# Performance work log

Measured on AMD Instinct MI355X. Metric: run time of the kernel, lower is better.

## Reference

```python
import jax, jax.numpy as jnp
import numpy as np

D_IN, D_K, D_V = 768, 128, 768


def setup_inputs() -> dict:
    key = jax.random.key(0)
    ks = jax.random.split(key, 7)
    x = jax.random.normal(ks[0], (4, 2048, D_IN), dtype=jnp.float32)
    s_in = 1.0 / np.sqrt(D_IN)
    Wq = jax.random.uniform(ks[1], (D_IN, D_K), minval=-s_in, maxval=s_in, dtype=jnp.float32)
    bq = jax.random.uniform(ks[2], (D_K,), minval=-s_in, maxval=s_in, dtype=jnp.float32)
    Wk = jax.random.uniform(ks[3], (D_IN, D_K), minval=-s_in, maxval=s_in, dtype=jnp.float32)
    bk = jax.random.uniform(ks[4], (D_K,), minval=-s_in, maxval=s_in, dtype=jnp.float32)
    Wv = jax.random.uniform(ks[5], (D_IN, D_V), minval=-s_in, maxval=s_in, dtype=jnp.float32)
    bv = jax.random.uniform(ks[6], (D_V,), minval=-s_in, maxval=s_in, dtype=jnp.float32)
    return {"x": x, "Wq": Wq, "bq": bq, "Wk": Wk, "bk": bk, "Wv": Wv, "bv": bv}


def reference(x, Wq, bq, Wk, bk, Wv, bv):
    # q,k: [b,t,d_k]; v: [b,t,d_v]
    q = jnp.einsum('bti,ik->btk', x, Wq) + bq
    k = jnp.einsum('bti,ik->btk', x, Wk) + bk
    v = jnp.einsum('bti,iv->btv', x, Wv) + bv
    scale = 1.0 / jnp.sqrt(jnp.asarray(D_K, dtype=jnp.float32))
    scores = jnp.einsum('bqk,btk->bqt', q, k) * scale  # [b,t,t]
    attn = jax.nn.softmax(scores, axis=-1)
    return jnp.einsum('bqt,btv->bqv', attn, v)
```

## Files before the change

### kernel.cpp

```cpp
#include <hip/hip_runtime.h>
#include <stdint.h>

typedef unsigned short u16;
typedef __attribute__((ext_vector_type(8))) short short8;
typedef __attribute__((ext_vector_type(4))) float f32x4;

#define BATCH 4
#define SEQ   2048
#define DIN   768
#define DK    128
#define DV    768
#define MTOT  (BATCH*SEQ)
#define NQKV  1024

__device__ __forceinline__ u16 f2bf(float f) {
  union { float f; uint32_t u; } v; v.f = f;
  uint32_t r = v.u + 0x7FFFu + ((v.u >> 16) & 1u);
  return (u16)(r >> 16);
}
__device__ __forceinline__ float bf2f(u16 h) {
  union { uint32_t u; float f; } v; v.u = ((uint32_t)h) << 16;
  return v.f;
}

__global__ void pack_bias(const float* __restrict__ bq, const float* __restrict__ bk,
                          const float* __restrict__ bv, float* __restrict__ biasP) {
  const float qs = 0.088388347648318447f;
  int n = blockIdx.x * 256 + threadIdx.x;
  if (n >= NQKV) return;
  biasP[n] = (n < DK) ? bq[n] * qs : (n < 2*DK ? bk[n - DK] : bv[n - 2*DK]);
}

__global__ __launch_bounds__(256) void pack_weight_t(const float* __restrict__ W,
                                                     u16* __restrict__ dst, int ldw, float sc) {
  __shared__ u16 tile[64][72];
  int i0 = blockIdx.x * 64;
  int n0 = blockIdx.y * 64;
  int tid = threadIdx.x;
  int tr = tid >> 2;
  int tc = (tid & 3) * 16;
  const float* src = W + (size_t)(i0 + tr) * ldw + n0 + tc;
  u16 o[16];
#pragma unroll
  for (int u = 0; u < 16; u += 4) {
    float4 v = *(const float4*)(src + u);
    o[u] = f2bf(v.x * sc); o[u+1] = f2bf(v.y * sc); o[u+2] = f2bf(v.z * sc); o[u+3] = f2bf(v.w * sc);
  }
  *(uint4*)&tile[tr][tc]     = *(const uint4*)&o[0];
  *(uint4*)&tile[tr][tc + 8] = *(const uint4*)&o[8];
  __syncthreads();
  u16 tmp[16];
#pragma unroll
  for (int u = 0; u < 16; ++u) tmp[u] = tile[tc + u][tr];
  u16* d = dst + (size_t)(n0 + tr) * DIN + i0 + tc;
  *(uint4*)d       = *(const uint4*)&tmp[0];
  *(uint4*)(d + 8) = *(const uint4*)&tmp[8];
}

__global__ void convert_x(const float* __restrict__ x, u16* __restrict__ xb) {
  int i = (blockIdx.x * blockDim.x + threadIdx.x) * 4;
  float4 v = *(const float4*)(x + i);
  u16 o[4] = { f2bf(v.x), f2bf(v.y), f2bf(v.z), f2bf(v.w) };
  *(uint2*)(xb + i) = *(const uint2*)o;
}

template<int MODE, int NJ>
__global__ __launch_bounds__(512, 4) void gemm_nt(
    const u16* __restrict__ A, int lda, long long sA,
    const u16* __restrict__ BT, int ldb, long long sB,
    void* __restrict__ C0, void* __restrict__ C1, int ldc, long long sC,
    int K, int gx, int gy, const float* __restrict__ bias,
    const float* __restrict__ rsum)
{
  __shared__ u16 As[2][128][64];
  __shared__ u16 Bs[2][NJ * 64][64];
  const int tid = threadIdx.x;
  const int l   = tid & 63;
  const int wid = tid >> 6;
  const int wm  = wid >> 2;
  const int wn  = wid & 3;

  const int nwg = gridDim.x;
  const int cpx = nwg >> 3;
  const int bid = blockIdx.x;
  const int wg  = (bid & 7) * cpx + (bid >> 3);
  const int z   = wg / (gx * gy);
  const int rem = wg - z * gx * gy;
  const int by  = rem / gx;
  const int bx  = rem - by * gx;
  const int m0  = bx * 128;
  const int n0  = by * (NJ * 64);

  A  += (size_t)z * (size_t)sA;
  BT += (size_t)z * (size_t)sB;

  f32x4 acc[4][NJ] = {};

  const int lr = l >> 3;
  const int lc = ((l & 7) ^ lr) * 8;

  const int CH = 2 + NJ;
  const int ca = wid * CH;
  auto STAGE = [&](int buf, int k0) {
#pragma unroll
    for (int i = 0; i < CH; ++i) {
      int c = ca + i;
      if (c < 16) {
        const u16* src = A + (size_t)(m0 + c * 8 + lr) * lda + k0 + lc;
        __builtin_amdgcn_global_load_lds(
            (const __attribute__((address_space(1))) unsigned int*)src,
            (__attribute__((address_space(3))) unsigned int*)&As[buf][c * 8][0],
            16, 0, 0);
      } else {
        int cb = c - 16;
        const u16* src = BT + (size_t)(n0 + cb * 8 + lr) * ldb + k0 + lc;
        __builtin_amdgcn_global_load_lds(
            (const __attribute__((address_space(1))) unsigned int*)src,
            (__attribute__((address_space(3))) unsigned int*)&Bs[buf][cb * 8][0],
            16, 0, 0);
      }
    }
  };

  STAGE(0, 0);
  __syncthreads();

  int cur = 0;
  for (int k0 = 0; k0 < K; k0 += 64) {
    if (k0 + 64 < K) STAGE(cur ^ 1, k0 + 64);
#pragma unroll
    for (int ks = 0; ks < 2; ++ks) {
      short8 af[4], bg[NJ];
#pragma unroll
      for (int i = 0; i < 4; ++i) {
        int row  = wm * 64 + i * 16 + (l & 15);
        int slot = (ks * 4 + (l >> 4)) ^ (row & 7);
        af[i] = *(const short8*)&As[cur][row][slot * 8];
      }
#pragma unroll
      for (int j = 0; j < NJ; ++j) {
        int row  = wn * (NJ * 16) + j * 16 + (l & 15);
        int slot = (ks * 4 + (l >> 4)) ^ (row & 7);
        bg[j] = *(const short8*)&Bs[cur][row][slot * 8];
      }
#pragma unroll
      for (int i = 0; i < 4; ++i)
#pragma unroll
        for (int j = 0; j < NJ; ++j)
          acc[i][j] = __builtin_amdgcn_mfma_f32_16x16x32_bf16(af[i], bg[j], acc[i][j], 0, 0, 0);
    }
    __syncthreads();
    cur ^= 1;
  }

  const int rbase = (l >> 4) * 4;
  const int cl    = l & 15;
#pragma unroll
  for (int i = 0; i < 4; ++i) {
#pragma unroll
    for (int j = 0; j < NJ; ++j) {
      int col = n0 + wn * (NJ * 16) + j * 16 + cl;
      int row0 = m0 + wm * 64 + i * 16 + rbase;
      if (MODE == 0) {
#pragma unroll
        for (int q = 0; q < 4; ++q) {
          float rs = rsum[(size_t)z * SEQ + row0 + q];
          ((float*)C0)[(size_t)z * (size_t)sC + (size_t)(row0 + q) * ldc + col] = acc[i][j][q] * rs;
        }
      } else if (MODE == 1) {
#pragma unroll
        for (int q = 0; q < 4; ++q)
          ((u16*)C0)[(size_t)z * (size_t)sC + (size_t)(row0 + q) * ldc + col] = f2bf(__expf(acc[i][j][q]));
      } else {
        float bv_ = bias[col];
        if (n0 < 256) {
#pragma unroll
          for (int q = 0; q < 4; ++q)
            ((u16*)C0)[(size_t)(row0 + q) * 256 + col] = f2bf(acc[i][j][q] + bv_);
        } else {
          int b = row0 >> 11, t = row0 & 2047;
          u16 o[4];
#pragma unroll
          for (int q = 0; q < 4; ++q) o[q] = f2bf(acc[i][j][q] + bv_);
          *(uint2*)&((u16*)C1)[((size_t)b * DV + (col - 256)) * SEQ + t] = *(const uint2*)o;
        }
      }
    }
  }
}

__global__ __launch_bounds__(256) void rowsum_inv(const u16* __restrict__ P, float* __restrict__ rinv) {
  int row = blockIdx.x * 4 + (threadIdx.x >> 6);
  int l   = threadIdx.x & 63;
  const u16* p = P + (size_t)row * SEQ;
  float s = 0.0f;
#pragma unroll
  for (int c = 0; c < 4; ++c) {
    uint4 d = *(const uint4*)(p + l * 8 + c * 512);
    const u16* u = (const u16*)&d;
#pragma unroll
    for (int e = 0; e < 8; ++e) s += bf2f(u[e]);
  }
#pragma unroll
  for (int sft = 32; sft; sft >>= 1) s += __shfl_xor(s, sft, 64);
  if (l == 0) rinv[row] = 1.0f / s;
}

extern "C" void kernel_launch(void* const* d_in, const int* in_sizes, int n_in,
                              void* d_out, int out_size, void* d_ws, size_t ws_size,
                              hipStream_t stream) {
  const float* x  = (const float*)d_in[0];
  const float* Wq = (const float*)d_in[1];
  const float* bq = (const float*)d_in[2];
  const float* Wk = (const float*)d_in[3];
  const float* bk = (const float*)d_in[4];
  const float* Wv = (const float*)d_in[5];
  const float* bv = (const float*)d_in[6];
  float* out = (float*)d_out;

  size_t off = 0;
  auto alloc = [&](size_t bytes) -> void* {
    void* p = (char*)d_ws + off;
    off += (bytes + 255) & ~(size_t)255;
    return p;
  };
  u16*   xb    = (u16*)alloc((size_t)MTOT * DIN * 2);
  u16*   WbT   = (u16*)alloc((size_t)NQKV * DIN * 2);
  float* biasP = (float*)alloc(NQKV * 4);
  u16*   qk    = (u16*)alloc((size_t)MTOT * 256 * 2);
  u16*   vT    = (u16*)alloc((size_t)BATCH * DV * SEQ * 2);
  u16*   P     = (u16*)alloc((size_t)BATCH * SEQ * SEQ * 2);
  float* rinv  = (float*)alloc((size_t)MTOT * 4);
  if (off > ws_size) return;

  const float qs = 0.088388347648318447f;

  pack_bias<<<dim3(4), dim3(256), 0, stream>>>(bq, bk, bv, biasP);
  pack_weight_t<<<dim3(DIN/64, DK/64), dim3(256), 0, stream>>>(Wq, WbT, DK, qs);
  pack_weight_t<<<dim3(DIN/64, DK/64), dim3(256), 0, stream>>>(Wk, WbT + (size_t)DK*DIN, DK, 1.0f);
  pack_weight_t<<<dim3(DIN/64, DV/64), dim3(256), 0, stream>>>(Wv, WbT + (size_t)2*DK*DIN, DV, 1.0f);
  convert_x<<<dim3((MTOT * DIN / 4) / 256), dim3(256), 0, stream>>>(x, xb);

  gemm_nt<2, 2><<<dim3(64 * 8), dim3(512), 0, stream>>>(
      xb, DIN, 0, WbT, DIN, 0, qk, vT, 0, 0, DIN, 64, 8, biasP, nullptr);

  gemm_nt<1, 2><<<dim3(16 * 16 * BATCH), dim3(512), 0, stream>>>(
      qk, 256, (long long)SEQ * 256,
      qk + DK, 256, (long long)SEQ * 256,
      P, nullptr, SEQ, (long long)SEQ * SEQ, DK, 16, 16, nullptr, nullptr);

  rowsum_inv<<<dim3(MTOT / 4), dim3(256), 0, stream>>>(P, rinv);

  gemm_nt<0, 3><<<dim3(16 * 4 * BATCH), dim3(512), 0, stream>>>(
      P, SEQ, (long long)SEQ * SEQ,
      vT, SEQ, (long long)DV * SEQ,
      out, nullptr, DV, (long long)SEQ * DV, SEQ, 16, 4, nullptr, rinv);
}
```

Before: 98.72 us.

## Fold softmax row sums into PV GEMM via ones-MFMA and merge pack kernels

Drops the separate rowsum_inv pass over the P matrix. Row sums are now computed inside the PV GEMM by an extra MFMA against a vector of bf16 ones, and the output is normalised in the epilogue. The QK^T exp step gets its own single-shot kernel that loads the full K=128 tile without double buffering. The three weight-pack launches and the bias-pack launch are merged into one kernel. The intent is to avoid re-reading the 32MB P buffer and to cut launch overhead, at the cost of extra MFMA work in the main GEMM.

```diff
diff --git a/kernel.cpp b/kernel.cpp
--- a/kernel.cpp
+++ b/kernel.cpp
@@ -23,20 +23,25 @@
   return v.f;
 }
 
-__global__ void pack_bias(const float* __restrict__ bq, const float* __restrict__ bk,
-                          const float* __restrict__ bv, float* __restrict__ biasP) {
+__global__ __launch_bounds__(256) void pack_all(
+    const float* __restrict__ Wq, const float* __restrict__ bq,
+    const float* __restrict__ Wk, const float* __restrict__ bk,
+    const float* __restrict__ Wv, const float* __restrict__ bv,
+    u16* __restrict__ WbT, float* __restrict__ biasP) {
   const float qs = 0.088388347648318447f;
-  int n = blockIdx.x * 256 + threadIdx.x;
-  if (n >= NQKV) return;
-  biasP[n] = (n < DK) ? bq[n] * qs : (n < 2*DK ? bk[n - DK] : bv[n - 2*DK]);
-}
-
-__global__ __launch_bounds__(256) void pack_weight_t(const float* __restrict__ W,
-                                                     u16* __restrict__ dst, int ldw, float sc) {
   __shared__ u16 tile[64][72];
+  int y = blockIdx.y;
+  const float* W; u16* dst; int ldw, nb; float sc;
+  if (y < 2)      { W = Wq; dst = WbT;                       ldw = DK; sc = qs;   nb = y;     }
+  else if (y < 4) { W = Wk; dst = WbT + (size_t)DK * DIN;    ldw = DK; sc = 1.0f; nb = y - 2; }
+  else            { W = Wv; dst = WbT + (size_t)2*DK * DIN;  ldw = DV; sc = 1.0f; nb = y - 4; }
   int i0 = blockIdx.x * 64;
-  int n0 = blockIdx.y * 64;
+  int n0 = nb * 64;
   int tid = threadIdx.x;
+  if (blockIdx.x == 0 && y == 0) {
+    for (int n = tid; n < NQKV; n += 256)
+      biasP[n] = (n < DK) ? bq[n] * qs : (n < 2*DK ? bk[n - DK] : bv[n - 2*DK]);
+  }
   int tr = tid >> 2;
   int tc = (tid & 3) * 16;
   const float* src = W + (size_t)(i0 + tr) * ldw + n0 + tc;
@@ -69,8 +74,7 @@
     const u16* __restrict__ A, int lda, long long sA,
     const u16* __restrict__ BT, int ldb, long long sB,
     void* __restrict__ C0, void* __restrict__ C1, int ldc, long long sC,
-    int K, int gx, int gy, const float* __restrict__ bias,
-    const float* __restrict__ rsum)
+    int K, int gx, int gy, const float* __restrict__ bias)
 {
   __shared__ u16 As[2][128][64];
   __shared__ u16 Bs[2][NJ * 64][64];
@@ -95,6 +99,8 @@
   BT += (size_t)z * (size_t)sB;
 
   f32x4 acc[4][NJ] = {};
+  f32x4 accO[4] = {};
+  const short8 kOnes = {16256,16256,16256,16256,16256,16256,16256,16256};
 
   const int lr = l >> 3;
   const int lc = ((l & 7) ^ lr) * 8;
@@ -148,6 +154,11 @@
 #pragma unroll
         for (int j = 0; j < NJ; ++j)
           acc[i][j] = __builtin_amdgcn_mfma_f32_16x16x32_bf16(af[i], bg[j], acc[i][j], 0, 0, 0);
+      if (MODE == 0) {
+#pragma unroll
+        for (int i = 0; i < 4; ++i)
+          accO[i] = __builtin_amdgcn_mfma_f32_16x16x32_bf16(af[i], kOnes, accO[i], 0, 0, 0);
+      }
     }
     __syncthreads();
     cur ^= 1;
@@ -157,20 +168,19 @@
   const int cl    = l & 15;
 #pragma unroll
   for (int i = 0; i < 4; ++i) {
+    f32x4 rs;
+    if (MODE == 0) {
+#pragma unroll
+      for (int q = 0; q < 4; ++q) rs[q] = 1.0f / accO[i][q];
+    }
 #pragma unroll
     for (int j = 0; j < NJ; ++j) {
       int col = n0 + wn * (NJ * 16) + j * 16 + cl;
       int row0 = m0 + wm * 64 + i * 16 + rbase;
       if (MODE == 0) {
 #pragma unroll
-        for (int q = 0; q < 4; ++q) {
-          float rs = rsum[(size_t)z * SEQ + row0 + q];
-          ((float*)C0)[(size_t)z * (size_t)sC + (size_t)(row0 + q) * ldc + col] = acc[i][j][q] * rs;
-        }
-      } else if (MODE == 1) {
-#pragma unroll
         for (int q = 0; q < 4; ++q)
-          ((u16*)C0)[(size_t)z * (size_t)sC + (size_t)(row0 + q) * ldc + col] = f2bf(__expf(acc[i][j][q]));
+          ((float*)C0)[(size_t)z * (size_t)sC + (size_t)(row0 + q) * ldc + col] = acc[i][j][q] * rs[q];
       } else {
         float bv_ = bias[col];
         if (n0 < 256) {
@@ -189,21 +199,93 @@
   }
 }
 
-__global__ __launch_bounds__(256) void rowsum_inv(const u16* __restrict__ P, float* __restrict__ rinv) {
-  int row = blockIdx.x * 4 + (threadIdx.x >> 6);
-  int l   = threadIdx.x & 63;
-  const u16* p = P + (size_t)row * SEQ;
-  float s = 0.0f;
-#pragma unroll
-  for (int c = 0; c < 4; ++c) {
-    uint4 d = *(const uint4*)(p + l * 8 + c * 512);
-    const u16* u = (const u16*)&d;
-#pragma unroll
-    for (int e = 0; e < 8; ++e) s += bf2f(u[e]);
-  }
-#pragma unroll
-  for (int sft = 32; sft; sft >>= 1) s += __shfl_xor(s, sft, 64);
-  if (l == 0) rinv[row] = 1.0f / s;
+__global__ __launch_bounds__(512, 4) void sgemm_exp(
+    const u16* __restrict__ qk, u16* __restrict__ P)
+{
+  __shared__ u16 As[128][128];
+  __shared__ u16 Bs[128][128];
+  const int tid = threadIdx.x;
+  const int l   = tid & 63;
+  const int wid = tid >> 6;
+  const int wm  = wid >> 2;
+  const int wn  = wid & 3;
+
+  const int nwg = gridDim.x;
+  const int cpx = nwg >> 3;
+  const int bid = blockIdx.x;
+  const int wg  = (bid & 7) * cpx + (bid >> 3);
+  const int z   = wg >> 8;
+  const int rem = wg & 255;
+  const int by  = rem >> 4;
+  const int bx  = rem & 15;
+  const int m0  = bx * 128;
+  const int n0  = by * 128;
+
+  const u16* A  = qk + (size_t)z * SEQ * 256;
+  const u16* BT = qk + DK + (size_t)z * SEQ * 256;
+
+  const int rin  = l >> 4;
+  const int s16  = l & 15;
+#pragma unroll
+  for (int i = 0; i < 8; ++i) {
+    int c = wid * 8 + i;
+    if (c < 32) {
+      int r = c * 4 + rin;
+      int gs = s16 ^ (r & 7);
+      const u16* src = A + (size_t)(m0 + r) * 256 + gs * 8;
+      __builtin_amdgcn_global_load_lds(
+          (const __attribute__((address_space(1))) unsigned int*)src,
+          (__attribute__((address_space(3))) unsigned int*)&As[c * 4][0],
+          16, 0, 0);
+    } else {
+      int cb = c - 32;
+      int r = cb * 4 + rin;
+      int gs = s16 ^ (r & 7);
+      const u16* src = BT + (size_t)(n0 + r) * 256 + gs * 8;
+      __builtin_amdgcn_global_load_lds(
+          (const __attribute__((address_space(1))) unsigned int*)src,
+          (__attribute__((address_space(3))) unsigned int*)&Bs[cb * 4][0],
+          16, 0, 0);
+    }
+  }
+  __syncthreads();
+
+  f32x4 acc[4][2] = {};
+#pragma unroll
+  for (int ks = 0; ks < 4; ++ks) {
+    short8 af[4], bg[2];
+#pragma unroll
+    for (int i = 0; i < 4; ++i) {
+      int row  = wm * 64 + i * 16 + (l & 15);
+      int slot = (ks * 4 + (l >> 4)) ^ (row & 7);
+      af[i] = *(const short8*)&As[row][slot * 8];
+    }
+#pragma unroll
+    for (int j = 0; j < 2; ++j) {
+      int row  = wn * 32 + j * 16 + (l & 15);
+      int slot = (ks * 4 + (l >> 4)) ^ (row & 7);
+      bg[j] = *(const short8*)&Bs[row][slot * 8];
+    }
+#pragma unroll
+    for (int i = 0; i < 4; ++i)
+#pragma unroll
+      for (int j = 0; j < 2; ++j)
+        acc[i][j] = __builtin_amdgcn_mfma_f32_16x16x32_bf16(af[i], bg[j], acc[i][j], 0, 0, 0);
+  }
+
+  const int rbase = (l >> 4) * 4;
+  const int cl    = l & 15;
+  u16* Pz = P + (size_t)z * SEQ * SEQ;
+#pragma unroll
+  for (int i = 0; i < 4; ++i)
+#pragma unroll
+    for (int j = 0; j < 2; ++j) {
+      int col  = n0 + wn * 32 + j * 16 + cl;
+      int row0 = m0 + wm * 64 + i * 16 + rbase;
+#pragma unroll
+      for (int q = 0; q < 4; ++q)
+        Pz[(size_t)(row0 + q) * SEQ + col] = f2bf(__expf(acc[i][j][q]));
+    }
 }
 
 extern "C" void kernel_launch(void* const* d_in, const int* in_sizes, int n_in,
@@ -230,29 +312,18 @@
   u16*   qk    = (u16*)alloc((size_t)MTOT * 256 * 2);
   u16*   vT    = (u16*)alloc((size_t)BATCH * DV * SEQ * 2);
   u16*   P     = (u16*)alloc((size_t)BATCH * SEQ * SEQ * 2);
-  float* rinv  = (float*)alloc((size_t)MTOT * 4);
   if (off > ws_size) return;
 
-  const float qs = 0.088388347648318447f;
-
-  pack_bias<<<dim3(4), dim3(256), 0, stream>>>(bq, bk, bv, biasP);
-  pack_weight_t<<<dim3(DIN/64, DK/64), dim3(256), 0, stream>>>(Wq, WbT, DK, qs);
-  pack_weight_t<<<dim3(DIN/64, DK/64), dim3(256), 0, stream>>>(Wk, WbT + (size_t)DK*DIN, DK, 1.0f);
-  pack_weight_t<<<dim3(DIN/64, DV/64), dim3(256), 0, stream>>>(Wv, WbT + (size_t)2*DK*DIN, DV, 1.0f);
+  pack_all<<<dim3(DIN/64, 16), dim3(256), 0, stream>>>(Wq, bq, Wk, bk, Wv, bv, WbT, biasP);
   convert_x<<<dim3((MTOT * DIN / 4) / 256), dim3(256), 0, stream>>>(x, xb);
 
   gemm_nt<2, 2><<<dim3(64 * 8), dim3(512), 0, stream>>>(
-      xb, DIN, 0, WbT, DIN, 0, qk, vT, 0, 0, DIN, 64, 8, biasP, nullptr);
-
-  gemm_nt<1, 2><<<dim3(16 * 16 * BATCH), dim3(512), 0, stream>>>(
-      qk, 256, (long long)SEQ * 256,
-      qk + DK, 256, (long long)SEQ * 256,
-      P, nullptr, SEQ, (long long)SEQ * SEQ, DK, 16, 16, nullptr, nullptr);
-
-  rowsum_inv<<<dim3(MTOT / 4), dim3(256), 0, stream>>>(P, rinv);
+      xb, DIN, 0, WbT, DIN, 0, qk, vT, 0, 0, DIN, 64, 8, biasP);
+
+  sgemm_exp<<<dim3(16 * 16 * BATCH), dim3(512), 0, stream>>>(qk, P);
 
   gemm_nt<0, 3><<<dim3(16 * 4 * BATCH), dim3(512), 0, stream>>>(
       P, SEQ, (long long)SEQ * SEQ,
       vT, SEQ, (long long)DV * SEQ,
-      out, nullptr, DV, (long long)SEQ * DV, SEQ, 16, 4, nullptr, rinv);
-}
+      out, nullptr, DV, (long long)SEQ * DV, SEQ, 16, 4, nullptr);
+}
```

New measurement: 86.55 us. 1.14x faster.
